# Performance work log

Hardware: AMD Instinct MI355X
Metric: run time of the kernel (lower is better)

Reference implementation:

```python
import jax, jax.numpy as jnp
import numpy as np
from jax import lax

B, S, H, I, E, TOP_K = 4, 4096, 2048, 1024, 8, 2


def setup_inputs() -> dict:
    key = jax.random.key(0)
    k1, k2, k3, k4, k5 = jax.random.split(key, 5)
    scale = 0.02  # realistic init scale so router logits are well-conditioned
    return {
        "x": jax.random.normal(k1, (B, S, H), dtype=jnp.float32),
        "gate_w": jax.random.normal(k2, (E, H), dtype=jnp.float32) * scale,
        "wg": jax.random.normal(k3, (E, H, I), dtype=jnp.float32) * scale,
        "wu": jax.random.normal(k4, (E, H, I), dtype=jnp.float32) * scale,
        "wd": jax.random.normal(k5, (E, I, H), dtype=jnp.float32) * scale,
    }


def reference(x, gate_w, wg, wu, wd):
    b, s, h = x.shape
    xt = x.reshape(b * s, h)                      # [T, H]
    router_logits = xt @ gate_w.T                 # [T, E]
    probs = jax.nn.softmax(router_logits, axis=-1)
    topk_w, topk_idx = lax.top_k(probs, TOP_K)    # [T, K]
    T = xt.shape[0]
    # combine[t, e] = routing weight of expert e for token t (0 if not in top-k)
    combine = jnp.zeros((T, E), xt.dtype).at[
        jnp.arange(T)[:, None], topk_idx
    ].set(topk_w)

    # scan over experts; each step is one grouped SwiGLU MLP over all tokens,
    # weighted by the (mostly-zero) combine column -> identical math to the
    # torch gather/index_add dispatch.
    def step(acc, ew):
        wgi, wui, wdi, c = ew                     # [H,I],[H,I],[I,H],[T]
        hdn = jax.nn.silu(xt @ wgi) * (xt @ wui)  # [T, I]
        return acc + c[:, None] * (hdn @ wdi), None

    acc, _ = lax.scan(step, jnp.zeros_like(xt), (wg, wu, wd, combine.T))
    return acc.reshape(b, s, h), router_logits
```

## Files before the change

kernel.cpp:

```cpp
#include <hip/hip_runtime.h>

#define T_TOK 16384
#define H_DIM 2048
#define I_DIM 1024
#define E_NUM 8

static const size_t F_WGT = 0;
static const size_t F_WUT = 33554432ull;
static const size_t F_XH  = 67108864ull;
static const size_t F_Y2  = 0;
static const size_t F_WDT = 134217728ull;
static const size_t F_HDN = 167772160ull;
static const size_t F_TOK = 234881024ull;
static const size_t F_WT  = 235405312ull;
static const size_t F_IDX = 235929600ull;
static const size_t F_CNT = 236060672ull;

typedef float f32x4 __attribute__((ext_vector_type(4)));
typedef _Float16 f16x8 __attribute__((ext_vector_type(8)));
typedef _Float16 f16x4 __attribute__((ext_vector_type(4)));

__device__ __forceinline__ void gload_lds16(const void* g, void* l) {
  __builtin_amdgcn_global_load_lds(
      (const __attribute__((address_space(1))) unsigned int*)g,
      (__attribute__((address_space(3))) unsigned int*)l, 16, 0, 0);
}

__global__ __launch_bounds__(256) void wconv_kernel(
    const float* __restrict__ wg, const float* __restrict__ wu,
    const float* __restrict__ wd, _Float16* __restrict__ wgT,
    _Float16* __restrict__ wuT, _Float16* __restrict__ wdT) {
  const int bx = blockIdx.x;
  const int w = bx >> 12;
  const int r2 = bx & 4095;
  const int e = r2 >> 9;
  const int t = r2 & 511;

  const float* src;
  _Float16* dst;
  int R, C;
  if (w == 0)      { src = wg; dst = wgT; R = H_DIM; C = I_DIM; }
  else if (w == 1) { src = wu; dst = wuT; R = H_DIM; C = I_DIM; }
  else             { src = wd; dst = wdT; R = I_DIM; C = H_DIM; }
  src += (size_t)e * R * C;
  dst += (size_t)e * R * C;

  const int tiles_c = C >> 6;
  const int tr = t / tiles_c;
  const int tc = t % tiles_c;

  __shared__ float tile[64][65];
  const int tid = threadIdx.x;

#pragma unroll
  for (int c = 0; c < 4; ++c) {
    const int q = c * 256 + tid;
    const int row = q >> 4;
    const int col4 = (q & 15) * 4;
    const float4 v = *(const float4*)(src + (size_t)(tr * 64 + row) * C + tc * 64 + col4);
    tile[row][col4 + 0] = v.x;
    tile[row][col4 + 1] = v.y;
    tile[row][col4 + 2] = v.z;
    tile[row][col4 + 3] = v.w;
  }
  __syncthreads();
#pragma unroll
  for (int c = 0; c < 4; ++c) {
    const int q = c * 256 + tid;
    const int row = q >> 4;
    const int col4 = (q & 15) * 4;
    f16x4 o = { (_Float16)tile[col4 + 0][row], (_Float16)tile[col4 + 1][row],
                (_Float16)tile[col4 + 2][row], (_Float16)tile[col4 + 3][row] };
    *(f16x4*)(dst + (size_t)(tc * 64 + row) * R + tr * 64 + col4) = o;
  }
}

__global__ __launch_bounds__(256) void router_kernel(
    const float* __restrict__ x, const float* __restrict__ gw,
    float* __restrict__ logits, int* __restrict__ tok_list,
    float* __restrict__ wt_list, int* __restrict__ idx2,
    int* __restrict__ counts, _Float16* __restrict__ xh) {
  const int lane = threadIdx.x & 63;
  const int wave = threadIdx.x >> 6;
  const int t = blockIdx.x * 4 + wave;
  const float* xr = x + (size_t)t * H_DIM;

  float xv[32];
#pragma unroll
  for (int j = 0; j < 32; ++j) xv[j] = xr[lane + j * 64];

  _Float16* xhr = xh + (size_t)t * H_DIM;
#pragma unroll
  for (int j = 0; j < 32; ++j) xhr[lane + j * 64] = (_Float16)xv[j];

  float lg[E_NUM];
#pragma unroll
  for (int e = 0; e < E_NUM; ++e) {
    const float* gr = gw + e * H_DIM;
    float s = 0.f;
#pragma unroll
    for (int j = 0; j < 32; ++j) s += xv[j] * gr[lane + j * 64];
#pragma unroll
    for (int off = 32; off > 0; off >>= 1) s += __shfl_xor(s, off, 64);
    lg[e] = s;
  }

  if (lane == 0) {
#pragma unroll
    for (int e = 0; e < E_NUM; ++e) logits[(size_t)t * E_NUM + e] = lg[e];
    float mx = lg[0];
#pragma unroll
    for (int e = 1; e < E_NUM; ++e) mx = fmaxf(mx, lg[e]);
    float se = 0.f;
#pragma unroll
    for (int e = 0; e < E_NUM; ++e) se += expf(lg[e] - mx);
    int i1 = 0; float b1 = lg[0];
#pragma unroll
    for (int e = 1; e < E_NUM; ++e) { if (lg[e] > b1) { b1 = lg[e]; i1 = e; } }
    int i2 = -1; float b2 = -1e30f;
#pragma unroll
    for (int e = 0; e < E_NUM; ++e) { if (e != i1 && lg[e] > b2) { b2 = lg[e]; i2 = e; } }
    const float p1 = expf(b1 - mx) / se;
    const float p2 = expf(b2 - mx) / se;
    int pos = atomicAdd(&counts[i1], 1);
    tok_list[i1 * T_TOK + pos] = t;
    wt_list[i1 * T_TOK + pos] = p1;
    idx2[t * 2] = (i1 << 16) | pos;
    pos = atomicAdd(&counts[i2], 1);
    tok_list[i2 * T_TOK + pos] = t;
    wt_list[i2 * T_TOK + pos] = p2;
    idx2[t * 2 + 1] = (i2 << 16) | pos;
  }
}

__global__ __launch_bounds__(256) void gemm1_kernel(
    const _Float16* __restrict__ xh, const _Float16* __restrict__ wgT,
    const _Float16* __restrict__ wuT, const int* __restrict__ tok_list,
    const int* __restrict__ counts, _Float16* __restrict__ hdn) {
  const int bx = blockIdx.x;
  const int cb = bx & 7;
  const int rb = (bx >> 3) & 127;
  const int e = bx >> 10;
  const int n_e = counts[e];
  const int row0 = rb * 128;
  if (row0 >= n_e) return;
  int goff = 0;
#pragma unroll
  for (int j = 0; j < E_NUM; ++j) goff += (j < e) ? counts[j] : 0;
  const int rem = min(128, n_e - row0);

  __shared__ int toks[128];
  __shared__ __attribute__((aligned(16))) _Float16 As[2][128 * 32];
  __shared__ __attribute__((aligned(16))) _Float16 Bg[2][128 * 32];
  __shared__ __attribute__((aligned(16))) _Float16 Bu[2][128 * 32];

  const int tid = threadIdx.x;
  if (tid < 128) {
    int idx = row0 + tid;
    if (idx > n_e - 1) idx = n_e - 1;
    toks[tid] = tok_list[e * T_TOK + idx];
  }
  __syncthreads();

  const int lane = tid & 63;
  const int wid = tid >> 6;
  const int wr = (wid >> 1) * 64;
  const int wcl = (wid & 1) * 64;
  const int n0 = cb * 128;

  const _Float16* wgTe = wgT + ((size_t)e * I_DIM + n0) * H_DIM;
  const _Float16* wuTe = wuT + ((size_t)e * I_DIM + n0) * H_DIM;

  const _Float16* asrc[2];
  int bofs[2], dofs[2];
#pragma unroll
  for (int c = 0; c < 2; ++c) {
    const int q = c * 256 + tid;
    const int rr = q >> 2;
    const int ch = q & 3;
    const int sch = ch ^ ((rr >> 1) & 3);
    asrc[c] = xh + (size_t)toks[rr] * H_DIM + sch * 8;
    bofs[c] = rr * H_DIM + sch * 8;
    dofs[c] = q * 8;
  }

  const f32x4 z4 = {0.f, 0.f, 0.f, 0.f};
  f32x4 accg[4][4], accu[4][4];
#pragma unroll
  for (int m = 0; m < 4; ++m)
#pragma unroll
    for (int n = 0; n < 4; ++n) { accg[m][n] = z4; accu[m][n] = z4; }

  const int cl = lane & 15;
  const int kq = lane >> 4;

  int aoff[4], boffr[4];
#pragma unroll
  for (int m = 0; m < 4; ++m) {
    const int row = wr + m * 16 + cl;
    aoff[m] = row * 32 + ((kq ^ ((row >> 1) & 3)) * 8);
  }
#pragma unroll
  for (int n = 0; n < 4; ++n) {
    const int row = wcl + n * 16 + cl;
    boffr[n] = row * 32 + ((kq ^ ((row >> 1) & 3)) * 8);
  }

#pragma unroll
  for (int c = 0; c < 2; ++c) {
    gload_lds16(asrc[c], &As[0][0] + dofs[c]);
    gload_lds16(wgTe + bofs[c], &Bg[0][0] + dofs[c]);
    gload_lds16(wuTe + bofs[c], &Bu[0][0] + dofs[c]);
  }
  asm volatile("s_waitcnt vmcnt(0)" ::: "memory");
  __builtin_amdgcn_s_barrier();
  __builtin_amdgcn_sched_barrier(0);

  const int NK = H_DIM / 32;
  for (int t = 0; t < NK; ++t) {
    const int cur = t & 1;
    if (t + 1 < NK) {
      const int kn = (t + 1) * 32;
#pragma unroll
      for (int c = 0; c < 2; ++c) {
        gload_lds16(asrc[c] + kn, &As[cur ^ 1][0] + dofs[c]);
        gload_lds16(wgTe + bofs[c] + kn, &Bg[cur ^ 1][0] + dofs[c]);
        gload_lds16(wuTe + bofs[c] + kn, &Bu[cur ^ 1][0] + dofs[c]);
      }
    }
    const _Float16* Ac = &As[cur][0];
    const _Float16* Gc = &Bg[cur][0];
    const _Float16* Uc = &Bu[cur][0];
    f16x8 af[4], bg[4], bu[4];
#pragma unroll
    for (int m = 0; m < 4; ++m) af[m] = *(const f16x8*)(Ac + aoff[m]);
#pragma unroll
    for (int n = 0; n < 4; ++n) {
      bg[n] = *(const f16x8*)(Gc + boffr[n]);
      bu[n] = *(const f16x8*)(Uc + boffr[n]);
    }
#pragma unroll
    for (int m = 0; m < 4; ++m)
#pragma unroll
      for (int n = 0; n < 4; ++n) {
        accg[m][n] = __builtin_amdgcn_mfma_f32_16x16x32_f16(af[m], bg[n], accg[m][n], 0, 0, 0);
        accu[m][n] = __builtin_amdgcn_mfma_f32_16x16x32_f16(af[m], bu[n], accu[m][n], 0, 0, 0);
      }
    asm volatile("s_waitcnt vmcnt(0)" ::: "memory");
    __builtin_amdgcn_s_barrier();
    __builtin_amdgcn_sched_barrier(0);
  }

  const int rq = lane >> 4;
#pragma unroll
  for (int m = 0; m < 4; ++m) {
#pragma unroll
    for (int r = 0; r < 4; ++r) {
      const int row = wr + m * 16 + rq * 4 + r;
      if (row < rem) {
        const size_t grow = (size_t)(goff + row0 + row);
#pragma unroll
        for (int n = 0; n < 4; ++n) {
          const float g = accg[m][n][r];
          const float u = accu[m][n][r];
          const float h = g / (1.f + __expf(-g)) * u;
          hdn[grow * I_DIM + n0 + wcl + n * 16 + cl] = (_Float16)h;
        }
      }
    }
  }
}

__global__ __launch_bounds__(256) void gemm2_kernel(
    const _Float16* __restrict__ hdn, const _Float16* __restrict__ wdT,
    const int* __restrict__ tok_list, const float* __restrict__ wt_list,
    const int* __restrict__ counts, _Float16* __restrict__ y2) {
  const int bx = blockIdx.x;
  const int nb = bx & 15;
  const int rb = (bx >> 4) & 127;
  const int e = bx >> 11;
  const int n_e = counts[e];
  const int row0 = rb * 128;
  if (row0 >= n_e) return;
  int goff = 0;
#pragma unroll
  for (int j = 0; j < E_NUM; ++j) goff += (j < e) ? counts[j] : 0;
  const int rem = min(128, n_e - row0);

  __shared__ float wts[128];
  __shared__ __attribute__((aligned(16))) _Float16 As[2][128 * 32];
  __shared__ __attribute__((aligned(16))) _Float16 Bs[2][128 * 32];

  const int tid = threadIdx.x;
  if (tid < 128) {
    int idx = row0 + tid;
    const bool valid = (idx < n_e);
    wts[tid] = valid ? wt_list[e * T_TOK + min(idx, n_e - 1)] : 0.f;
  }
  __syncthreads();

  const int lane = tid & 63;
  const int wid = tid >> 6;
  const int wr = (wid >> 1) * 64;
  const int wcl = (wid & 1) * 64;
  const int h0 = nb * 128;

  const _Float16* wdTe = wdT + ((size_t)e * H_DIM + h0) * I_DIM;
  const _Float16* hdnb = hdn + (size_t)(goff + row0) * I_DIM;

  const _Float16* asrc[2];
  int bofs[2], dofs[2];
#pragma unroll
  for (int c = 0; c < 2; ++c) {
    const int q = c * 256 + tid;
    const int rr = q >> 2;
    const int ch = q & 3;
    const int sch = ch ^ ((rr >> 1) & 3);
    const int rrc = min(rr, rem - 1);
    asrc[c] = hdnb + (size_t)rrc * I_DIM + sch * 8;
    bofs[c] = rr * I_DIM + sch * 8;
    dofs[c] = q * 8;
  }

  const f32x4 z4 = {0.f, 0.f, 0.f, 0.f};
  f32x4 acc[4][4];
#pragma unroll
  for (int m = 0; m < 4; ++m)
#pragma unroll
    for (int n = 0; n < 4; ++n) acc[m][n] = z4;

  const int cl = lane & 15;
  const int kq = lane >> 4;

  int aoff[4], boffr[4];
#pragma unroll
  for (int m = 0; m < 4; ++m) {
    const int row = wr + m * 16 + cl;
    aoff[m] = row * 32 + ((kq ^ ((row >> 1) & 3)) * 8);
  }
#pragma unroll
  for (int n = 0; n < 4; ++n) {
    const int row = wcl + n * 16 + cl;
    boffr[n] = row * 32 + ((kq ^ ((row >> 1) & 3)) * 8);
  }

#pragma unroll
  for (int c = 0; c < 2; ++c) {
    gload_lds16(asrc[c], &As[0][0] + dofs[c]);
    gload_lds16(wdTe + bofs[c], &Bs[0][0] + dofs[c]);
  }
  asm volatile("s_waitcnt vmcnt(0)" ::: "memory");
  __builtin_amdgcn_s_barrier();
  __builtin_amdgcn_sched_barrier(0);

  const int NK = I_DIM / 32;
  for (int t = 0; t < NK; ++t) {
    const int cur = t & 1;
    if (t + 1 < NK) {
      const int kn = (t + 1) * 32;
#pragma unroll
      for (int c = 0; c < 2; ++c) {
        gload_lds16(asrc[c] + kn, &As[cur ^ 1][0] + dofs[c]);
        gload_lds16(wdTe + bofs[c] + kn, &Bs[cur ^ 1][0] + dofs[c]);
      }
    }
    const _Float16* Ac = &As[cur][0];
    const _Float16* Bc = &Bs[cur][0];
    f16x8 af[4], bf[4];
#pragma unroll
    for (int m = 0; m < 4; ++m) af[m] = *(const f16x8*)(Ac + aoff[m]);
#pragma unroll
    for (int n = 0; n < 4; ++n) bf[n] = *(const f16x8*)(Bc + boffr[n]);
#pragma unroll
    for (int m = 0; m < 4; ++m)
#pragma unroll
      for (int n = 0; n < 4; ++n)
        acc[m][n] = __builtin_amdgcn_mfma_f32_16x16x32_f16(af[m], bf[n], acc[m][n], 0, 0, 0);
    asm volatile("s_waitcnt vmcnt(0)" ::: "memory");
    __builtin_amdgcn_s_barrier();
    __builtin_amdgcn_sched_barrier(0);
  }

  const int rq = lane >> 4;
#pragma unroll
  for (int m = 0; m < 4; ++m) {
#pragma unroll
    for (int r = 0; r < 4; ++r) {
      const int row = wr + m * 16 + rq * 4 + r;
      if (row < rem) {
        const float w = wts[row];
        _Float16* yrow = y2 + (size_t)(goff + row0 + row) * H_DIM + h0 + wcl;
#pragma unroll
        for (int n = 0; n < 4; ++n)
          yrow[n * 16 + cl] = (_Float16)(acc[m][n][r] * w);
      }
    }
  }
}

__global__ __launch_bounds__(256) void combine_kernel(
    const _Float16* __restrict__ y2, const int* __restrict__ idx2,
    const int* __restrict__ counts, float* __restrict__ out) {
  const int t = blockIdx.x;
  int pref[E_NUM];
  int run = 0;
#pragma unroll
  for (int e = 0; e < E_NUM; ++e) { pref[e] = run; run += counts[e]; }
  const int p0 = idx2[t * 2];
  const int p1 = idx2[t * 2 + 1];
  const size_t r0 = (size_t)(pref[p0 >> 16] + (p0 & 0xFFFF)) * H_DIM;
  const size_t r1 = (size_t)(pref[p1 >> 16] + (p1 & 0xFFFF)) * H_DIM;
  const int o = threadIdx.x * 8;
  const f16x8 a = *(const f16x8*)(y2 + r0 + o);
  const f16x8 b = *(const f16x8*)(y2 + r1 + o);
  float* orow = out + (size_t)t * H_DIM + o;
  float4 lo = { (float)a[0] + (float)b[0], (float)a[1] + (float)b[1],
                (float)a[2] + (float)b[2], (float)a[3] + (float)b[3] };
  float4 hi = { (float)a[4] + (float)b[4], (float)a[5] + (float)b[5],
                (float)a[6] + (float)b[6], (float)a[7] + (float)b[7] };
  *(float4*)orow = lo;
  *(float4*)(orow + 4) = hi;
}

extern "C" void kernel_launch(void* const* d_in, const int* in_sizes, int n_in,
                              void* d_out, int out_size, void* d_ws, size_t ws_size,
                              hipStream_t stream) {
  (void)in_sizes; (void)n_in; (void)out_size; (void)ws_size;
  const float* x      = (const float*)d_in[0];
  const float* gate_w = (const float*)d_in[1];
  const float* wg     = (const float*)d_in[2];
  const float* wu     = (const float*)d_in[3];
  const float* wd     = (const float*)d_in[4];
  float* out0 = (float*)d_out;
  float* out1 = out0 + (size_t)T_TOK * H_DIM;

  char* ws = (char*)d_ws;
  _Float16* wgT = (_Float16*)(ws + F_WGT);
  _Float16* wuT = (_Float16*)(ws + F_WUT);
  _Float16* xh  = (_Float16*)(ws + F_XH);
  _Float16* y2  = (_Float16*)(ws + F_Y2);
  _Float16* wdT = (_Float16*)(ws + F_WDT);
  _Float16* hdn = (_Float16*)(ws + F_HDN);
  int* tok_list = (int*)(ws + F_TOK);
  float* wt_list = (float*)(ws + F_WT);
  int* idx2 = (int*)(ws + F_IDX);
  int* counts = (int*)(ws + F_CNT);

  hipMemsetAsync(counts, 0, 64, stream);
  wconv_kernel<<<12288, 256, 0, stream>>>(wg, wu, wd, wgT, wuT, wdT);
  router_kernel<<<T_TOK / 4, 256, 0, stream>>>(x, gate_w, out1, tok_list, wt_list, idx2, counts, xh);
  gemm1_kernel<<<E_NUM * 128 * 8, 256, 0, stream>>>(xh, wgT, wuT, tok_list, counts, hdn);
  gemm2_kernel<<<E_NUM * 128 * 16, 256, 0, stream>>>(hdn, wdT, tok_list, wt_list, counts, y2);
  combine_kernel<<<T_TOK, 256, 0, stream>>>(y2, idx2, counts, out0);
}
```

Measured before the change: 1.450 ms.

## Triple-buffer LDS pipeline and remap block order across XCDs in both GEMMs

Both expert GEMM kernels move from double to triple-buffered LDS, prefetching two K-tiles ahead and waiting only on the older group of global->LDS loads (vmcnt(6)/vmcnt(4)) instead of draining all loads every iteration. This keeps more memory traffic in flight to hide load latency behind MFMA work. The block index is also remapped so that blocks dispatched round-robin across the 8 XCDs get contiguous work ranges, improving L2 reuse of weight and activation tiles. The cost is 50% more LDS per block (about 72KB for gemm1), which may lower occupancy.

```diff
diff --git a/kernel.cpp b/kernel.cpp
--- a/kernel.cpp
+++ b/kernel.cpp
@@ -137,7 +137,10 @@
     const _Float16* __restrict__ xh, const _Float16* __restrict__ wgT,
     const _Float16* __restrict__ wuT, const int* __restrict__ tok_list,
     const int* __restrict__ counts, _Float16* __restrict__ hdn) {
-  const int bx = blockIdx.x;
+  const int cpx = (E_NUM * 128 * 8) >> 3;
+  int bx = blockIdx.x;
+  bx = (bx & 7) * cpx + (bx >> 3);
+
   const int cb = bx & 7;
   const int rb = (bx >> 3) & 127;
   const int e = bx >> 10;
@@ -150,9 +153,9 @@
   const int rem = min(128, n_e - row0);
 
   __shared__ int toks[128];
-  __shared__ __attribute__((aligned(16))) _Float16 As[2][128 * 32];
-  __shared__ __attribute__((aligned(16))) _Float16 Bg[2][128 * 32];
-  __shared__ __attribute__((aligned(16))) _Float16 Bu[2][128 * 32];
+  __shared__ __attribute__((aligned(16))) _Float16 As[3][128 * 32];
+  __shared__ __attribute__((aligned(16))) _Float16 Bg[3][128 * 32];
+  __shared__ __attribute__((aligned(16))) _Float16 Bu[3][128 * 32];
 
   const int tid = threadIdx.x;
   if (tid < 128) {
@@ -212,20 +215,27 @@
     gload_lds16(wgTe + bofs[c], &Bg[0][0] + dofs[c]);
     gload_lds16(wuTe + bofs[c], &Bu[0][0] + dofs[c]);
   }
-  asm volatile("s_waitcnt vmcnt(0)" ::: "memory");
+#pragma unroll
+  for (int c = 0; c < 2; ++c) {
+    gload_lds16(asrc[c] + 32, &As[1][0] + dofs[c]);
+    gload_lds16(wgTe + bofs[c] + 32, &Bg[1][0] + dofs[c]);
+    gload_lds16(wuTe + bofs[c] + 32, &Bu[1][0] + dofs[c]);
+  }
+  asm volatile("s_waitcnt vmcnt(6)" ::: "memory");
   __builtin_amdgcn_s_barrier();
   __builtin_amdgcn_sched_barrier(0);
 
   const int NK = H_DIM / 32;
+  int cur = 0;
   for (int t = 0; t < NK; ++t) {
-    const int cur = t & 1;
-    if (t + 1 < NK) {
-      const int kn = (t + 1) * 32;
+    const int nx2 = (cur >= 1) ? cur - 1 : cur + 2;
+    if (t + 2 < NK) {
+      const int kn = (t + 2) * 32;
 #pragma unroll
       for (int c = 0; c < 2; ++c) {
-        gload_lds16(asrc[c] + kn, &As[cur ^ 1][0] + dofs[c]);
-        gload_lds16(wgTe + bofs[c] + kn, &Bg[cur ^ 1][0] + dofs[c]);
-        gload_lds16(wuTe + bofs[c] + kn, &Bu[cur ^ 1][0] + dofs[c]);
+        gload_lds16(asrc[c] + kn, &As[nx2][0] + dofs[c]);
+        gload_lds16(wgTe + bofs[c] + kn, &Bg[nx2][0] + dofs[c]);
+        gload_lds16(wuTe + bofs[c] + kn, &Bu[nx2][0] + dofs[c]);
       }
     }
     const _Float16* Ac = &As[cur][0];
@@ -246,9 +256,11 @@
         accg[m][n] = __builtin_amdgcn_mfma_f32_16x16x32_f16(af[m], bg[n], accg[m][n], 0, 0, 0);
         accu[m][n] = __builtin_amdgcn_mfma_f32_16x16x32_f16(af[m], bu[n], accu[m][n], 0, 0, 0);
       }
-    asm volatile("s_waitcnt vmcnt(0)" ::: "memory");
+    if (t + 2 < NK) asm volatile("s_waitcnt vmcnt(6)" ::: "memory");
+    else            asm volatile("s_waitcnt vmcnt(0)" ::: "memory");
     __builtin_amdgcn_s_barrier();
     __builtin_amdgcn_sched_barrier(0);
+    cur = (cur == 2) ? 0 : cur + 1;
   }
 
   const int rq = lane >> 4;
@@ -275,7 +287,10 @@
     const _Float16* __restrict__ hdn, const _Float16* __restrict__ wdT,
     const int* __restrict__ tok_list, const float* __restrict__ wt_list,
     const int* __restrict__ counts, _Float16* __restrict__ y2) {
-  const int bx = blockIdx.x;
+  const int cpx = (E_NUM * 128 * 16) >> 3;
+  int bx = blockIdx.x;
+  bx = (bx & 7) * cpx + (bx >> 3);
+
   const int nb = bx & 15;
   const int rb = (bx >> 4) & 127;
   const int e = bx >> 11;
@@ -288,8 +303,8 @@
   const int rem = min(128, n_e - row0);
 
   __shared__ float wts[128];
-  __shared__ __attribute__((aligned(16))) _Float16 As[2][128 * 32];
-  __shared__ __attribute__((aligned(16))) _Float16 Bs[2][128 * 32];
+  __shared__ __attribute__((aligned(16))) _Float16 As[3][128 * 32];
+  __shared__ __attribute__((aligned(16))) _Float16 Bs[3][128 * 32];
 
   const int tid = threadIdx.x;
   if (tid < 128) {
@@ -349,19 +364,25 @@
     gload_lds16(asrc[c], &As[0][0] + dofs[c]);
     gload_lds16(wdTe + bofs[c], &Bs[0][0] + dofs[c]);
   }
-  asm volatile("s_waitcnt vmcnt(0)" ::: "memory");
+#pragma unroll
+  for (int c = 0; c < 2; ++c) {
+    gload_lds16(asrc[c] + 32, &As[1][0] + dofs[c]);
+    gload_lds16(wdTe + bofs[c] + 32, &Bs[1][0] + dofs[c]);
+  }
+  asm volatile("s_waitcnt vmcnt(4)" ::: "memory");
   __builtin_amdgcn_s_barrier();
   __builtin_amdgcn_sched_barrier(0);
 
   const int NK = I_DIM / 32;
+  int cur = 0;
   for (int t = 0; t < NK; ++t) {
-    const int cur = t & 1;
-    if (t + 1 < NK) {
-      const int kn = (t + 1) * 32;
+    const int nx2 = (cur >= 1) ? cur - 1 : cur + 2;
+    if (t + 2 < NK) {
+      const int kn = (t + 2) * 32;
 #pragma unroll
       for (int c = 0; c < 2; ++c) {
-        gload_lds16(asrc[c] + kn, &As[cur ^ 1][0] + dofs[c]);
-        gload_lds16(wdTe + bofs[c] + kn, &Bs[cur ^ 1][0] + dofs[c]);
+        gload_lds16(asrc[c] + kn, &As[nx2][0] + dofs[c]);
+        gload_lds16(wdTe + bofs[c] + kn, &Bs[nx2][0] + dofs[c]);
       }
     }
     const _Float16* Ac = &As[cur][0];
@@ -376,9 +397,11 @@
 #pragma unroll
       for (int n = 0; n < 4; ++n)
         acc[m][n] = __builtin_amdgcn_mfma_f32_16x16x32_f16(af[m], bf[n], acc[m][n], 0, 0, 0);
-    asm volatile("s_waitcnt vmcnt(0)" ::: "memory");
+    if (t + 2 < NK) asm volatile("s_waitcnt vmcnt(4)" ::: "memory");
+    else            asm volatile("s_waitcnt vmcnt(0)" ::: "memory");
     __builtin_amdgcn_s_barrier();
     __builtin_amdgcn_sched_barrier(0);
+    cur = (cur == 2) ? 0 : cur + 1;
   }
 
   const int rq = lane >> 4;
```

Result: slower. 1.510 ms (+4.1%).
